# Kernel optimization log

Measured on AMD Instinct MI355X. Metric: run time of the kernel, lower is better.

Reference implementation:

```python
import jax, jax.numpy as jnp
import numpy as np

H, I, E, TOPK = 1024, 4096, 8, 2
B, S = 2, 2048


def setup_inputs() -> dict:
    key = jax.random.key(0)
    ks = jax.random.split(key, 6)
    x = jax.random.normal(ks[0], (B, S, H), dtype=jnp.float32)
    expert_indices = jax.random.randint(ks[1], (B, S, TOPK), 0, E)
    expert_weights = jax.random.uniform(ks[2], (B, S, TOPK), dtype=jnp.float32)
    gate_proj = jax.random.normal(ks[3], (E, I, H), dtype=jnp.float32) * 0.02
    up_proj = jax.random.normal(ks[4], (E, I, H), dtype=jnp.float32) * 0.02
    down_proj = jax.random.normal(ks[5], (E, H, I), dtype=jnp.float32) * 0.02
    return {"x": x, "expert_indices": expert_indices, "expert_weights": expert_weights,
            "gate_proj": gate_proj, "up_proj": up_proj, "down_proj": down_proj}


def reference(x, expert_indices, expert_weights, gate_proj, up_proj, down_proj):
    b, s, h = x.shape
    xf = x.reshape(-1, h)                      # [T, H]
    ei = expert_indices.reshape(-1, expert_indices.shape[-1])   # [T, K]
    ew = expert_weights.reshape(-1, expert_weights.shape[-1])   # [T, K]
    n_experts = gate_proj.shape[0]
    out = jnp.zeros_like(xf)
    for e in range(n_experts):
        # combined routing weight of this expert per token (sum over topk slots)
        w_e = jnp.sum(jnp.where(ei == e, ew, 0.0), axis=-1)     # [T]
        g = xf @ gate_proj[e].T                # [T, I]
        u = xf @ up_proj[e].T                  # [T, I]
        inter = jax.nn.silu(g) * u             # fused SiLU*mul
        out = out + w_e[:, None] * (inter @ down_proj[e].T)     # weighted scatter-add
    return out.reshape(b, s, h)
```

## Files before the change

### kernel.cpp

```cpp
#include <hip/hip_runtime.h>
#include <cstdint>
#include <cstddef>

#define H_DIM 1024
#define I_DIM 4096
#define E_NUM 8
#define TOPK  2
#define T_NUM 4096
#define NROWS (T_NUM * TOPK)
#define BK    32

typedef _Float16 half8 __attribute__((ext_vector_type(8)));
typedef float    f32x4 __attribute__((ext_vector_type(4)));

__device__ __forceinline__ void async_copy16(void* lds, const void* g)
{
    __builtin_amdgcn_global_load_lds(
        (__attribute__((address_space(1))) unsigned int*)g,
        (__attribute__((address_space(3))) unsigned int*)lds,
        16 , 0 , 0 );
}


#define NX4 (T_NUM * H_DIM / 4)
#define NW4 (E_NUM * I_DIM * H_DIM / 4)
__global__ void cvt_all(const float* __restrict__ x,  const float* __restrict__ gp,
                        const float* __restrict__ up, const float* __restrict__ dp,
                        _Float16* __restrict__ xh, _Float16* __restrict__ wg,
                        _Float16* __restrict__ wu, _Float16* __restrict__ wd)
{
    int i = blockIdx.x * blockDim.x + threadIdx.x;
    const int total = NX4 + 3 * NW4;
    if (i >= total) return;
    const float* s; _Float16* d; int j;
    if (i < NX4)              { s = x;  d = xh; j = i; }
    else if (i < NX4 + NW4)   { s = gp; d = wg; j = i - NX4; }
    else if (i < NX4 + 2*NW4) { s = up; d = wu; j = i - NX4 - NW4; }
    else                      { s = dp; d = wd; j = i - NX4 - 2*NW4; }
    float4 v = reinterpret_cast<const float4*>(s)[j];
    union { _Float16 h[4]; unsigned long long u; } o;
    o.h[0] = (_Float16)v.x; o.h[1] = (_Float16)v.y;
    o.h[2] = (_Float16)v.z; o.h[3] = (_Float16)v.w;
    reinterpret_cast<unsigned long long*>(d)[j] = o.u;
}

__global__ void route_all(const int* __restrict__ ei, const float* __restrict__ ew,
                          int* __restrict__ offs,
                          int* __restrict__ token_of_row, float* __restrict__ weight_of_row)
{
    __shared__ int cnt[E_NUM];
    __shared__ int cur[E_NUM];
    const int t = (int)threadIdx.x;
    if (t < E_NUM) cnt[t] = 0;
    __syncthreads();
    for (int s = t; s < NROWS; s += (int)blockDim.x) atomicAdd(&cnt[ei[s]], 1);
    __syncthreads();
    if (t == 0) {
        int acc = 0;
        for (int e = 0; e < E_NUM; ++e) { offs[e] = acc; cur[e] = acc; acc += cnt[e]; }
        offs[E_NUM] = acc;
    }
    __syncthreads();
    for (int s = t; s < NROWS; s += (int)blockDim.x) {
        int e = ei[s];
        int r = atomicAdd(&cur[e], 1);
        token_of_row[r]  = s >> 1;
        weight_of_row[r] = ew[s];
    }
}

__global__ __launch_bounds__(256) void gateup_gemm(
    const _Float16* __restrict__ xh,
    const _Float16* __restrict__ Wg,
    const _Float16* __restrict__ Wu,
    const int*      __restrict__ token_of_row,
    const int*      __restrict__ offs,
    _Float16*       __restrict__ inter)
{
    const int e = blockIdx.z;
    const int seg_start = offs[e], seg_end = offs[e + 1];
    const int m0 = seg_start + (int)blockIdx.y * 128;
    if (m0 >= seg_end) return;
    const int n0 = (int)blockIdx.x * 64;

    __shared__ _Float16 Ash[128 * BK];
    __shared__ _Float16 Bgs[64 * BK];
    __shared__ _Float16 Bus[64 * BK];

    const int tid  = (int)threadIdx.x;
    const int lane = tid & 63, wid = tid >> 6;
    const int wm = wid >> 1, wn = wid & 1;

    const int c   = lane & 3;
    const int rl  = lane >> 2;
    const int frl = (rl & 3) ^ (rl >> 2);
    const int gc  = c ^ frl;

    const _Float16* pA[2];
    _Float16* lA[2];
#pragma unroll
    for (int j = 0; j < 2; ++j) {
        int q = 2 * wid + j;
        int r = m0 + q * 16 + rl;
        if (r > seg_end - 1) r = seg_end - 1;
        int tok = token_of_row[r];
        pA[j] = xh + (size_t)tok * H_DIM + gc * 8;
        lA[j] = &Ash[q * 16 * BK];
    }
    const int brow = wid * 16 + rl;
    const _Float16* pBg = Wg + ((size_t)e * I_DIM + n0 + brow) * H_DIM + gc * 8;
    const _Float16* pBu = Wu + ((size_t)e * I_DIM + n0 + brow) * H_DIM + gc * 8;
    _Float16* lBg = &Bgs[wid * 16 * BK];
    _Float16* lBu = &Bus[wid * 16 * BK];

    f32x4 accg[4][2], accu[4][2];
#pragma unroll
    for (int i = 0; i < 4; ++i)
#pragma unroll
        for (int j = 0; j < 2; ++j) {
            accg[i][j] = (f32x4){0.f, 0.f, 0.f, 0.f};
            accu[i][j] = (f32x4){0.f, 0.f, 0.f, 0.f};
        }

    const int fm = lane & 15, kq = lane >> 4;
    const int fsw = (fm & 3) ^ ((fm >> 2) & 3);
    const int rdo = (kq ^ fsw) * 8;

    for (int kt = 0; kt < H_DIM / BK; ++kt) {
        const int ko = kt * BK;
        __syncthreads();
        async_copy16(lA[0], pA[0] + ko);
        async_copy16(lA[1], pA[1] + ko);
        async_copy16(lBg,   pBg   + ko);
        async_copy16(lBu,   pBu   + ko);
        __syncthreads();

        half8 a[4], bg[2], bu[2];
#pragma unroll
        for (int i = 0; i < 4; ++i)
            a[i] = *(const half8*)&Ash[(wm * 64 + i * 16 + fm) * BK + rdo];
#pragma unroll
        for (int j = 0; j < 2; ++j) {
            bg[j] = *(const half8*)&Bgs[(wn * 32 + j * 16 + fm) * BK + rdo];
            bu[j] = *(const half8*)&Bus[(wn * 32 + j * 16 + fm) * BK + rdo];
        }
#pragma unroll
        for (int i = 0; i < 4; ++i)
#pragma unroll
            for (int j = 0; j < 2; ++j) {
                accg[i][j] = __builtin_amdgcn_mfma_f32_16x16x32_f16(a[i], bg[j], accg[i][j], 0, 0, 0);
                accu[i][j] = __builtin_amdgcn_mfma_f32_16x16x32_f16(a[i], bu[j], accu[i][j], 0, 0, 0);
            }
    }

#pragma unroll
    for (int i = 0; i < 4; ++i) {
#pragma unroll
        for (int reg = 0; reg < 4; ++reg) {
            int r = m0 + wm * 64 + i * 16 + kq * 4 + reg;
            if (r < seg_end) {
#pragma unroll
                for (int j = 0; j < 2; ++j) {
                    int col = n0 + wn * 32 + j * 16 + fm;
                    float g = accg[i][j][reg];
                    float u = accu[i][j][reg];
                    float sv = (g / (1.f + __expf(-g))) * u;
                    inter[(size_t)r * I_DIM + col] = (_Float16)sv;
                }
            }
        }
    }
}

__global__ __launch_bounds__(256) void down_gemm(
    const _Float16* __restrict__ inter,
    const _Float16* __restrict__ Wd,
    const int*      __restrict__ token_of_row,
    const float*    __restrict__ weight_of_row,
    const int*      __restrict__ offs,
    float*          __restrict__ out)
{
    const int e = blockIdx.z;
    const int seg_start = offs[e], seg_end = offs[e + 1];
    const int m0 = seg_start + (int)blockIdx.y * 128;
    if (m0 >= seg_end) return;
    const int n0 = (int)blockIdx.x * 128;

    __shared__ _Float16 Ash[128 * BK];
    __shared__ _Float16 Bsh[128 * BK];

    const int tid  = (int)threadIdx.x;
    const int lane = tid & 63, wid = tid >> 6;
    const int wm = wid >> 1, wn = wid & 1;
    const int c   = lane & 3;
    const int rl  = lane >> 2;
    const int frl = (rl & 3) ^ (rl >> 2);
    const int gc  = c ^ frl;

    const _Float16* pA[2]; _Float16* lA[2];
    const _Float16* pB[2]; _Float16* lB[2];
#pragma unroll
    for (int j = 0; j < 2; ++j) {
        int q = 2 * wid + j;
        int row_in = q * 16 + rl;
        int r = m0 + row_in;
        if (r > seg_end - 1) r = seg_end - 1;
        pA[j] = inter + (size_t)r * I_DIM + gc * 8;
        lA[j] = &Ash[q * 16 * BK];
        int n = n0 + row_in;
        pB[j] = Wd + ((size_t)e * H_DIM + n) * I_DIM + gc * 8;
        lB[j] = &Bsh[q * 16 * BK];
    }

    f32x4 acc[4][4];
#pragma unroll
    for (int i = 0; i < 4; ++i)
#pragma unroll
        for (int j = 0; j < 4; ++j) acc[i][j] = (f32x4){0.f, 0.f, 0.f, 0.f};

    const int fm = lane & 15, kq = lane >> 4;
    const int fsw = (fm & 3) ^ ((fm >> 2) & 3);
    const int rdo = (kq ^ fsw) * 8;

    for (int kt = 0; kt < I_DIM / BK; ++kt) {
        const int ko = kt * BK;
        __syncthreads();
        async_copy16(lA[0], pA[0] + ko);
        async_copy16(lA[1], pA[1] + ko);
        async_copy16(lB[0], pB[0] + ko);
        async_copy16(lB[1], pB[1] + ko);
        __syncthreads();

        half8 a[4], b[4];
#pragma unroll
        for (int i = 0; i < 4; ++i)
            a[i] = *(const half8*)&Ash[(wm * 64 + i * 16 + fm) * BK + rdo];
#pragma unroll
        for (int j = 0; j < 4; ++j)
            b[j] = *(const half8*)&Bsh[(wn * 64 + j * 16 + fm) * BK + rdo];
#pragma unroll
        for (int i = 0; i < 4; ++i)
#pragma unroll
            for (int j = 0; j < 4; ++j)
                acc[i][j] = __builtin_amdgcn_mfma_f32_16x16x32_f16(a[i], b[j], acc[i][j], 0, 0, 0);
    }

#pragma unroll
    for (int i = 0; i < 4; ++i) {
#pragma unroll
        for (int reg = 0; reg < 4; ++reg) {
            int r = m0 + wm * 64 + i * 16 + kq * 4 + reg;
            if (r < seg_end) {
                float w = weight_of_row[r];
                int   t = token_of_row[r];
#pragma unroll
                for (int j = 0; j < 4; ++j) {
                    int col = n0 + wn * 64 + j * 16 + fm;
                    atomicAdd(&out[(size_t)t * H_DIM + col], w * acc[i][j][reg]);
                }
            }
        }
    }
}

extern "C" void kernel_launch(void* const* d_in, const int* in_sizes, int n_in,
                              void* d_out, int out_size, void* d_ws, size_t ws_size,
                              hipStream_t stream)
{
    const float* x  = (const float*)d_in[0];
    const int*   ei = (const int*)  d_in[1];
    const float* ew = (const float*)d_in[2];
    const float* gp = (const float*)d_in[3];
    const float* up = (const float*)d_in[4];
    const float* dp = (const float*)d_in[5];
    float* out = (float*)d_out;

    char* ws = (char*)d_ws;
    size_t o = 0;
    _Float16* xh    = (_Float16*)(ws + o); o += (size_t)T_NUM * H_DIM * 2;
    _Float16* Wg_h  = (_Float16*)(ws + o); o += (size_t)E_NUM * I_DIM * H_DIM * 2;
    _Float16* Wu_h  = (_Float16*)(ws + o); o += (size_t)E_NUM * I_DIM * H_DIM * 2;
    _Float16* Wd_h  = (_Float16*)(ws + o); o += (size_t)E_NUM * I_DIM * H_DIM * 2;
    _Float16* inter = (_Float16*)(ws + o); o += (size_t)NROWS * I_DIM * 2;
    int*   offs          = (int*)  (ws + o);
    int*   token_of_row  = (int*)  (ws + o + 256);
    float* weight_of_row = (float*)(ws + o + 256 + (size_t)NROWS * 4);
    size_t ws_need = o + 256 + (size_t)NROWS * 8;
    if (ws_size < ws_need) return;

    hipMemsetAsync(d_out, 0, (size_t)out_size * sizeof(float), stream);

    const int nt = 256;
    const int ncvt = NX4 + 3 * NW4;
    cvt_all<<<(ncvt + nt - 1) / nt, nt, 0, stream>>>(x, gp, up, dp, xh, Wg_h, Wu_h, Wd_h);

    route_all<<<1, 1024, 0, stream>>>(ei, ew, offs, token_of_row, weight_of_row);

    gateup_gemm<<<dim3(I_DIM / 64, NROWS / 128, E_NUM), 256, 0, stream>>>(
        xh, Wg_h, Wu_h, token_of_row, offs, inter);
    down_gemm<<<dim3(H_DIM / 128, NROWS / 128, E_NUM), 256, 0, stream>>>(
        inter, Wd_h, token_of_row, weight_of_row, offs, out);
}
```

Baseline: 713.4 us.

## Load fp32 expert weights directly in GEMMs and drop separate weight conversion pass

Removes the pre-pass that converted all gate, up and down weights to fp16 in global memory. The GEMM kernels now stream fp32 weight tiles into shared memory using a new 8-column XOR swizzle and convert them to fp16 while building MFMA fragments. This avoids a full read-and-write pass over all expert weights, at the cost of double-size weight tiles in LDS and extra conversion work inside the inner loop. The grid's row-block dimension is also cut to 16 per expert, which cuts early-exit blocks but assumes no expert receives more than 2048 routed rows.

```diff
diff --git a/kernel.cpp b/kernel.cpp
--- a/kernel.cpp
+++ b/kernel.cpp
@@ -9,6 +9,7 @@
 #define T_NUM 4096
 #define NROWS (T_NUM * TOPK)
 #define BK    32
+#define YMAX  16
 
 typedef _Float16 half8 __attribute__((ext_vector_type(8)));
 typedef float    f32x4 __attribute__((ext_vector_type(4)));
@@ -22,26 +23,26 @@
 }
 
 
+__device__ __forceinline__ half8 read_b_frag(const float* __restrict__ Brow, int kq, int sw8)
+{
+    const f32x4 lo = *(const f32x4*)(Brow + ((((2 * kq)     ^ sw8)) << 2));
+    const f32x4 hi = *(const f32x4*)(Brow + ((((2 * kq + 1) ^ sw8)) << 2));
+    half8 r;
+    r[0] = (_Float16)lo[0]; r[1] = (_Float16)lo[1]; r[2] = (_Float16)lo[2]; r[3] = (_Float16)lo[3];
+    r[4] = (_Float16)hi[0]; r[5] = (_Float16)hi[1]; r[6] = (_Float16)hi[2]; r[7] = (_Float16)hi[3];
+    return r;
+}
+
 #define NX4 (T_NUM * H_DIM / 4)
-#define NW4 (E_NUM * I_DIM * H_DIM / 4)
-__global__ void cvt_all(const float* __restrict__ x,  const float* __restrict__ gp,
-                        const float* __restrict__ up, const float* __restrict__ dp,
-                        _Float16* __restrict__ xh, _Float16* __restrict__ wg,
-                        _Float16* __restrict__ wu, _Float16* __restrict__ wd)
+__global__ void cvt_x(const float* __restrict__ x, _Float16* __restrict__ xh)
 {
     int i = blockIdx.x * blockDim.x + threadIdx.x;
-    const int total = NX4 + 3 * NW4;
-    if (i >= total) return;
-    const float* s; _Float16* d; int j;
-    if (i < NX4)              { s = x;  d = xh; j = i; }
-    else if (i < NX4 + NW4)   { s = gp; d = wg; j = i - NX4; }
-    else if (i < NX4 + 2*NW4) { s = up; d = wu; j = i - NX4 - NW4; }
-    else                      { s = dp; d = wd; j = i - NX4 - 2*NW4; }
-    float4 v = reinterpret_cast<const float4*>(s)[j];
+    if (i >= NX4) return;
+    float4 v = reinterpret_cast<const float4*>(x)[i];
     union { _Float16 h[4]; unsigned long long u; } o;
     o.h[0] = (_Float16)v.x; o.h[1] = (_Float16)v.y;
     o.h[2] = (_Float16)v.z; o.h[3] = (_Float16)v.w;
-    reinterpret_cast<unsigned long long*>(d)[j] = o.u;
+    reinterpret_cast<unsigned long long*>(xh)[i] = o.u;
 }
 
 __global__ void route_all(const int* __restrict__ ei, const float* __restrict__ ew,
@@ -71,8 +72,8 @@
 
 __global__ __launch_bounds__(256) void gateup_gemm(
     const _Float16* __restrict__ xh,
-    const _Float16* __restrict__ Wg,
-    const _Float16* __restrict__ Wu,
+    const float*    __restrict__ Wg,
+    const float*    __restrict__ Wu,
     const int*      __restrict__ token_of_row,
     const int*      __restrict__ offs,
     _Float16*       __restrict__ inter)
@@ -84,34 +85,43 @@
     const int n0 = (int)blockIdx.x * 64;
 
     __shared__ _Float16 Ash[128 * BK];
-    __shared__ _Float16 Bgs[64 * BK];
-    __shared__ _Float16 Bus[64 * BK];
+    __shared__ float    Bgs[64 * BK];
+    __shared__ float    Bus[64 * BK];
 
     const int tid  = (int)threadIdx.x;
     const int lane = tid & 63, wid = tid >> 6;
     const int wm = wid >> 1, wn = wid & 1;
 
-    const int c   = lane & 3;
-    const int rl  = lane >> 2;
-    const int frl = (rl & 3) ^ (rl >> 2);
-    const int gc  = c ^ frl;
+    const int c4   = lane & 3;
+    const int rl16 = lane >> 2;
+    const int frl  = (rl16 & 3) ^ (rl16 >> 2);
+    const int gc4  = c4 ^ frl;
+    const int c8  = lane & 7;
+    const int rl8 = lane >> 3;
+    const int gc8 = c8 ^ rl8;
 
     const _Float16* pA[2];
     _Float16* lA[2];
 #pragma unroll
     for (int j = 0; j < 2; ++j) {
         int q = 2 * wid + j;
-        int r = m0 + q * 16 + rl;
+        int r = m0 + q * 16 + rl16;
         if (r > seg_end - 1) r = seg_end - 1;
         int tok = token_of_row[r];
-        pA[j] = xh + (size_t)tok * H_DIM + gc * 8;
+        pA[j] = xh + (size_t)tok * H_DIM + gc4 * 8;
         lA[j] = &Ash[q * 16 * BK];
     }
-    const int brow = wid * 16 + rl;
-    const _Float16* pBg = Wg + ((size_t)e * I_DIM + n0 + brow) * H_DIM + gc * 8;
-    const _Float16* pBu = Wu + ((size_t)e * I_DIM + n0 + brow) * H_DIM + gc * 8;
-    _Float16* lBg = &Bgs[wid * 16 * BK];
-    _Float16* lBu = &Bus[wid * 16 * BK];
+    const float* pBg[2]; const float* pBu[2];
+    float* lBg[2]; float* lBu[2];
+#pragma unroll
+    for (int j = 0; j < 2; ++j) {
+        int q = 2 * wid + j;
+        int row = q * 8 + rl8;
+        pBg[j] = Wg + ((size_t)e * I_DIM + n0 + row) * H_DIM + gc8 * 4;
+        pBu[j] = Wu + ((size_t)e * I_DIM + n0 + row) * H_DIM + gc8 * 4;
+        lBg[j] = &Bgs[q * 8 * BK];
+        lBu[j] = &Bus[q * 8 * BK];
+    }
 
     f32x4 accg[4][2], accu[4][2];
 #pragma unroll
@@ -123,26 +133,29 @@
         }
 
     const int fm = lane & 15, kq = lane >> 4;
-    const int fsw = (fm & 3) ^ ((fm >> 2) & 3);
-    const int rdo = (kq ^ fsw) * 8;
+    const int fswA = (fm & 3) ^ ((fm >> 2) & 3);
+    const int rdoA = (kq ^ fswA) * 8;
+    const int sw8  = fm & 7;
 
     for (int kt = 0; kt < H_DIM / BK; ++kt) {
         const int ko = kt * BK;
         __syncthreads();
-        async_copy16(lA[0], pA[0] + ko);
-        async_copy16(lA[1], pA[1] + ko);
-        async_copy16(lBg,   pBg   + ko);
-        async_copy16(lBu,   pBu   + ko);
+        async_copy16(lA[0],  pA[0]  + ko);
+        async_copy16(lA[1],  pA[1]  + ko);
+        async_copy16(lBg[0], pBg[0] + ko);
+        async_copy16(lBg[1], pBg[1] + ko);
+        async_copy16(lBu[0], pBu[0] + ko);
+        async_copy16(lBu[1], pBu[1] + ko);
         __syncthreads();
 
         half8 a[4], bg[2], bu[2];
 #pragma unroll
         for (int i = 0; i < 4; ++i)
-            a[i] = *(const half8*)&Ash[(wm * 64 + i * 16 + fm) * BK + rdo];
+            a[i] = *(const half8*)&Ash[(wm * 64 + i * 16 + fm) * BK + rdoA];
 #pragma unroll
         for (int j = 0; j < 2; ++j) {
-            bg[j] = *(const half8*)&Bgs[(wn * 32 + j * 16 + fm) * BK + rdo];
-            bu[j] = *(const half8*)&Bus[(wn * 32 + j * 16 + fm) * BK + rdo];
+            bg[j] = read_b_frag(&Bgs[(wn * 32 + j * 16 + fm) * BK], kq, sw8);
+            bu[j] = read_b_frag(&Bus[(wn * 32 + j * 16 + fm) * BK], kq, sw8);
         }
 #pragma unroll
         for (int i = 0; i < 4; ++i)
@@ -174,7 +187,7 @@
 
 __global__ __launch_bounds__(256) void down_gemm(
     const _Float16* __restrict__ inter,
-    const _Float16* __restrict__ Wd,
+    const float*    __restrict__ Wd,
     const int*      __restrict__ token_of_row,
     const float*    __restrict__ weight_of_row,
     const int*      __restrict__ offs,
@@ -187,29 +200,36 @@
     const int n0 = (int)blockIdx.x * 128;
 
     __shared__ _Float16 Ash[128 * BK];
-    __shared__ _Float16 Bsh[128 * BK];
+    __shared__ float    Bsh[128 * BK];
 
     const int tid  = (int)threadIdx.x;
     const int lane = tid & 63, wid = tid >> 6;
     const int wm = wid >> 1, wn = wid & 1;
-    const int c   = lane & 3;
-    const int rl  = lane >> 2;
-    const int frl = (rl & 3) ^ (rl >> 2);
-    const int gc  = c ^ frl;
+
+    const int c4   = lane & 3;
+    const int rl16 = lane >> 2;
+    const int frl  = (rl16 & 3) ^ (rl16 >> 2);
+    const int gc4  = c4 ^ frl;
+    const int c8  = lane & 7;
+    const int rl8 = lane >> 3;
+    const int gc8 = c8 ^ rl8;
 
     const _Float16* pA[2]; _Float16* lA[2];
-    const _Float16* pB[2]; _Float16* lB[2];
 #pragma unroll
     for (int j = 0; j < 2; ++j) {
         int q = 2 * wid + j;
-        int row_in = q * 16 + rl;
-        int r = m0 + row_in;
+        int r = m0 + q * 16 + rl16;
         if (r > seg_end - 1) r = seg_end - 1;
-        pA[j] = inter + (size_t)r * I_DIM + gc * 8;
+        pA[j] = inter + (size_t)r * I_DIM + gc4 * 8;
         lA[j] = &Ash[q * 16 * BK];
-        int n = n0 + row_in;
-        pB[j] = Wd + ((size_t)e * H_DIM + n) * I_DIM + gc * 8;
-        lB[j] = &Bsh[q * 16 * BK];
+    }
+    const float* pB[4]; float* lB[4];
+#pragma unroll
+    for (int j = 0; j < 4; ++j) {
+        int q = 4 * wid + j;
+        int row = q * 8 + rl8;
+        pB[j] = Wd + ((size_t)e * H_DIM + n0 + row) * I_DIM + gc8 * 4;
+        lB[j] = &Bsh[q * 8 * BK];
     }
 
     f32x4 acc[4][4];
@@ -219,25 +239,26 @@
         for (int j = 0; j < 4; ++j) acc[i][j] = (f32x4){0.f, 0.f, 0.f, 0.f};
 
     const int fm = lane & 15, kq = lane >> 4;
-    const int fsw = (fm & 3) ^ ((fm >> 2) & 3);
-    const int rdo = (kq ^ fsw) * 8;
+    const int fswA = (fm & 3) ^ ((fm >> 2) & 3);
+    const int rdoA = (kq ^ fswA) * 8;
+    const int sw8  = fm & 7;
 
     for (int kt = 0; kt < I_DIM / BK; ++kt) {
         const int ko = kt * BK;
         __syncthreads();
         async_copy16(lA[0], pA[0] + ko);
         async_copy16(lA[1], pA[1] + ko);
-        async_copy16(lB[0], pB[0] + ko);
-        async_copy16(lB[1], pB[1] + ko);
+#pragma unroll
+        for (int j = 0; j < 4; ++j) async_copy16(lB[j], pB[j] + ko);
         __syncthreads();
 
         half8 a[4], b[4];
 #pragma unroll
         for (int i = 0; i < 4; ++i)
-            a[i] = *(const half8*)&Ash[(wm * 64 + i * 16 + fm) * BK + rdo];
+            a[i] = *(const half8*)&Ash[(wm * 64 + i * 16 + fm) * BK + rdoA];
 #pragma unroll
         for (int j = 0; j < 4; ++j)
-            b[j] = *(const half8*)&Bsh[(wn * 64 + j * 16 + fm) * BK + rdo];
+            b[j] = read_b_frag(&Bsh[(wn * 64 + j * 16 + fm) * BK], kq, sw8);
 #pragma unroll
         for (int i = 0; i < 4; ++i)
 #pragma unroll
@@ -278,9 +299,6 @@
     char* ws = (char*)d_ws;
     size_t o = 0;
     _Float16* xh    = (_Float16*)(ws + o); o += (size_t)T_NUM * H_DIM * 2;
-    _Float16* Wg_h  = (_Float16*)(ws + o); o += (size_t)E_NUM * I_DIM * H_DIM * 2;
-    _Float16* Wu_h  = (_Float16*)(ws + o); o += (size_t)E_NUM * I_DIM * H_DIM * 2;
-    _Float16* Wd_h  = (_Float16*)(ws + o); o += (size_t)E_NUM * I_DIM * H_DIM * 2;
     _Float16* inter = (_Float16*)(ws + o); o += (size_t)NROWS * I_DIM * 2;
     int*   offs          = (int*)  (ws + o);
     int*   token_of_row  = (int*)  (ws + o + 256);
@@ -291,13 +309,12 @@
     hipMemsetAsync(d_out, 0, (size_t)out_size * sizeof(float), stream);
 
     const int nt = 256;
-    const int ncvt = NX4 + 3 * NW4;
-    cvt_all<<<(ncvt + nt - 1) / nt, nt, 0, stream>>>(x, gp, up, dp, xh, Wg_h, Wu_h, Wd_h);
+    cvt_x<<<(NX4 + nt - 1) / nt, nt, 0, stream>>>(x, xh);
 
     route_all<<<1, 1024, 0, stream>>>(ei, ew, offs, token_of_row, weight_of_row);
 
-    gateup_gemm<<<dim3(I_DIM / 64, NROWS / 128, E_NUM), 256, 0, stream>>>(
-        xh, Wg_h, Wu_h, token_of_row, offs, inter);
-    down_gemm<<<dim3(H_DIM / 128, NROWS / 128, E_NUM), 256, 0, stream>>>(
-        inter, Wd_h, token_of_row, weight_of_row, offs, out);
-}
+    gateup_gemm<<<dim3(I_DIM / 64, YMAX, E_NUM), 256, 0, stream>>>(
+        xh, gp, up, token_of_row, offs, inter);
+    down_gemm<<<dim3(H_DIM / 128, YMAX, E_NUM), 256, 0, stream>>>(
+        inter, dp, token_of_row, weight_of_row, offs, out);
+}
```

Result: slower. 738.4 us (+3.5%).
